# Optimization experiments

Measured on AMD Instinct MI355X. Metric: run time of the kernel, lower is better.

## Reference

```python
import jax, jax.numpy as jnp
import numpy as np
from jax import lax

N, T, E, A, D, S, O = 64, 2048, 512, 256, 512, 64, 80
R_ATT, R_FAC = 10, 2
H4 = 4 * D  # LSTM hidden size = 2048


def softsign(x):
    return x / (1.0 + jnp.abs(x))


def lstm_cell(x, h, c, Wih, Whh, bih, bhh):
    gates = x @ Wih.T + bih + h @ Whh.T + bhh
    i, f, g, o = jnp.split(gates, 4, axis=-1)  # torch gate order i,f,g,o
    c_new = jax.nn.sigmoid(f) * c + jax.nn.sigmoid(i) * jnp.tanh(g)
    h_new = jax.nn.sigmoid(o) * jnp.tanh(c_new)
    return h_new, c_new


def setup_inputs() -> dict:
    key = jax.random.key(0)
    ks = jax.random.split(key, 24)
    f = lambda k, shape, s=0.05: jax.random.normal(k, shape, dtype=jnp.float32) * s
    return {
        'input_enc': f(ks[0], (N, T, E), 1.0),
        'input_dec': f(ks[1], (N, O), 1.0),
        'spkr_vec': f(ks[2], (N, 1, S), 1.0),
        'speed': jax.random.uniform(ks[3], (N,), dtype=jnp.float32),
        'lengths_enc': jnp.full((N,), T, dtype=jnp.int32),
        'We': f(ks[4], (E, A)), 'be': jnp.zeros((A,), jnp.float32),
        'Ws': f(ks[5], (S, A)),
        'conv_w': f(ks[6], (A, 1, 31)),
        'w_proj': f(ks[7], (A,)), 'b_proj': jnp.zeros((), jnp.float32),
        'W_speed': f(ks[8], (A,)),
        'sp_W1': f(ks[9], (D,)), 'sp_b1': jnp.zeros((D,), jnp.float32),
        'sp_W2': f(ks[10], (D, E)), 'sp_b2': jnp.zeros((E,), jnp.float32),
        'pre_W1': f(ks[11], (O + S, 2 * D)), 'pre_b1': jnp.zeros((2 * D,), jnp.float32),
        'pre_W2': f(ks[12], (2 * D, D)), 'pre_b2': jnp.zeros((D,), jnp.float32),
        'Wih0': f(ks[13], (4 * H4, E + D + S)), 'Whh0': f(ks[14], (4 * H4, H4)),
        'bih0': jnp.zeros((4 * H4,), jnp.float32), 'bhh0': jnp.zeros((4 * H4,), jnp.float32),
        'Wih1': f(ks[15], (4 * H4, H4)), 'Whh1': f(ks[16], (4 * H4, H4)),
        'bih1': jnp.zeros((4 * H4,), jnp.float32), 'bhh1': jnp.zeros((4 * H4,), jnp.float32),
        'Wo': f(ks[17], (H4 + E, O * R_FAC)), 'bo': jnp.zeros((O * R_FAC,), jnp.float32),
    }


def _forward(input_enc, input_dec, spkr_vec, speed, lengths_enc,
             We, be, Ws, conv_w, w_proj, b_proj, W_speed,
             sp_W1, sp_b1, sp_W2, sp_b2,
             pre_W1, pre_b1, pre_W2, pre_b2,
             Wih0, Whh0, bih0, bhh0, Wih1, Whh1, bih1, bhh1, Wo, bo):
    n, t_enc, _ = input_enc.shape
    # first decoding step: previous attention = one-hot at t=0
    att0 = jnp.zeros((n, t_enc), jnp.float32).at[:, 0].set(1.0)
    bias_speed = (speed[:, None] * W_speed[None, :])[:, None, :]            # (N,1,A)
    bias_enc = softsign(jnp.einsum('nte,ea->nta', input_enc, We) + be)      # (N,T,A)
    bias_spkr = softsign(jnp.einsum('nse,ea->nsa', spkr_vec, Ws))           # (N,1,A)
    # prenet (dropout = identity at inference)
    x = jnp.concatenate([input_dec, spkr_vec[:, 0, :]], axis=-1)
    p = jax.nn.relu(jax.nn.relu(x @ pre_W1 + pre_b1) @ pre_W2 + pre_b2)     # (N,D)
    out_prenet = p[:, None, :]
    # location feature: conv1d(1->A, k=31, pad=15) over previous attention
    conv = lax.conv_general_dilated(att0[:, None, :], conv_w, (1,), [(15, 15)],
                                    dimension_numbers=('NCH', 'OIH', 'NCH'))
    conv = conv.transpose(0, 2, 1)                                          # (N,T,A)
    e = bias_enc + bias_spkr + conv + bias_speed                            # (N,T,A)
    # sliding-window mask around previous argmax, indices clamped to [0, len-1]
    m = jnp.argmax(att0, axis=1)                                            # (N,)
    L1 = (lengths_enc - 1).astype(m.dtype)
    i = jnp.arange(R_ATT)
    up = jnp.minimum(m[:, None] + i, L1[:, None])
    lo = jnp.minimum(jnp.maximum(m[:, None] - i, 0), L1[:, None])
    idx = jnp.concatenate([up, lo], axis=1)                                 # (N,2R)
    mask = jnp.zeros((n, t_enc), jnp.float32).at[jnp.arange(n)[:, None], idx].set(1.0)
    logit = jnp.einsum('nta,a->nt', jnp.tanh(e), w_proj) + b_proj           # (N,T)
    w = jnp.exp(logit - jnp.max(logit, axis=1, keepdims=True)) * mask
    att = w / jnp.maximum(jnp.sum(w, axis=1, keepdims=True), 1e-12)         # L1 normalize
    # speed-conditioned encoder shift
    sp = jnp.tanh(jax.nn.relu(speed[:, None] * sp_W1 + sp_b1) @ sp_W2 + sp_b2)  # (N,E)
    enc = input_enc + sp[:, None, :]
    context = jnp.einsum('nt,nte->ne', att, enc)[:, None, :]                # (N,1,E)
    in_lstm = jnp.concatenate([out_prenet, context, spkr_vec], axis=2)[:, 0, :]
    h0 = jnp.zeros((n, H4), jnp.float32)
    h1, _ = lstm_cell(in_lstm, h0, h0, Wih0, Whh0, bih0, bhh0)
    h2, _ = lstm_cell(h1, h0, h0, Wih1, Whh1, bih1, bhh1)
    dec_output = jnp.concatenate([h2[:, None, :], context], axis=2)         # (N,1,H4+E)
    output = (dec_output @ Wo + bo).reshape(n, R_FAC, -1)                   # (N,r,O)
    return output, context, dec_output


def reference(input_enc, input_dec, spkr_vec, speed, lengths_enc,
              We, be, Ws, conv_w, w_proj, b_proj, W_speed,
              sp_W1, sp_b1, sp_W2, sp_b2,
              pre_W1, pre_b1, pre_W2, pre_b2,
              Wih0, Whh0, bih0, bhh0, Wih1, Whh1, bih1, bhh1, Wo, bo):
    return _forward(input_enc, input_dec, spkr_vec, speed, lengths_enc,
                    We, be, Ws, conv_w, w_proj, b_proj, W_speed,
                    sp_W1, sp_b1, sp_W2, sp_b2,
                    pre_W1, pre_b1, pre_W2, pre_b2,
                    Wih0, Whh0, bih0, bhh0, Wih1, Whh1, bih1, bhh1, Wo, bo)
```

## Files before the change

### kernel.cpp

```cpp
#include <hip/hip_runtime.h>
#include <math.h>


__device__ __forceinline__ float sigmoidf_(float x){ return 1.0f/(1.0f+expf(-x)); }
__device__ __forceinline__ float softsignf_(float x){ return x/(1.0f+fabsf(x)); }


__global__ void hidden_kernel(const float* __restrict__ input_dec, const float* __restrict__ spkr,
                              const float* __restrict__ W, const float* __restrict__ b,
                              float* __restrict__ hid)
{
    const int n = blockIdx.x;
    const int j = blockIdx.y * 256 + threadIdx.x;
    float a0=0.f, a1=0.f, a2=0.f, a3=0.f;
    #pragma unroll 4
    for (int k = 0; k < 144; k += 4) {
        const float x0 = (k+0 < 80) ? input_dec[n*80 + k+0] : spkr[n*64 + (k+0-80)];
        const float x1 = (k+1 < 80) ? input_dec[n*80 + k+1] : spkr[n*64 + (k+1-80)];
        const float x2 = (k+2 < 80) ? input_dec[n*80 + k+2] : spkr[n*64 + (k+2-80)];
        const float x3 = (k+3 < 80) ? input_dec[n*80 + k+3] : spkr[n*64 + (k+3-80)];
        a0 = fmaf(x0, W[(k+0)*1024 + j], a0);
        a1 = fmaf(x1, W[(k+1)*1024 + j], a1);
        a2 = fmaf(x2, W[(k+2)*1024 + j], a2);
        a3 = fmaf(x3, W[(k+3)*1024 + j], a3);
    }
    hid[n*1024 + j] = fmaxf((a0+a1)+(a2+a3) + b[j], 0.f);
}

__global__ void sp_kernel(const float* __restrict__ speed, const float* __restrict__ sp_W1,
                          const float* __restrict__ sp_b1, const float* __restrict__ sp_W2,
                          const float* __restrict__ sp_b2, float* __restrict__ sp)
{
    const int n = blockIdx.x;
    const int j = blockIdx.y * 256 + threadIdx.x;
    const float s = speed[n];
    float a0=0.f, a1=0.f, a2=0.f, a3=0.f;
    #pragma unroll 4
    for (int d = 0; d < 512; d += 4) {
        const float r0 = fmaxf(fmaf(s, sp_W1[d+0], sp_b1[d+0]), 0.f);
        const float r1 = fmaxf(fmaf(s, sp_W1[d+1], sp_b1[d+1]), 0.f);
        const float r2 = fmaxf(fmaf(s, sp_W1[d+2], sp_b1[d+2]), 0.f);
        const float r3 = fmaxf(fmaf(s, sp_W1[d+3], sp_b1[d+3]), 0.f);
        a0 = fmaf(r0, sp_W2[(d+0)*512 + j], a0);
        a1 = fmaf(r1, sp_W2[(d+1)*512 + j], a1);
        a2 = fmaf(r2, sp_W2[(d+2)*512 + j], a2);
        a3 = fmaf(r3, sp_W2[(d+3)*512 + j], a3);
    }
    sp[n*512 + j] = tanhf((a0+a1)+(a2+a3) + sp_b2[j]);
}

__global__ void p_kernel(const float* __restrict__ hid, const float* __restrict__ W,
                         const float* __restrict__ b, float* __restrict__ xT0)
{
    const int n = blockIdx.x;
    const int j = blockIdx.y * 256 + threadIdx.x;
    const float* xr = hid + n*1024;
    float a0=0.f, a1=0.f, a2=0.f, a3=0.f;
    #pragma unroll 4
    for (int k = 0; k < 1024; k += 4) {
        a0 = fmaf(xr[k+0], W[(k+0)*512 + j], a0);
        a1 = fmaf(xr[k+1], W[(k+1)*512 + j], a1);
        a2 = fmaf(xr[k+2], W[(k+2)*512 + j], a2);
        a3 = fmaf(xr[k+3], W[(k+3)*512 + j], a3);
    }
    xT0[j*64 + n] = fmaxf((a0+a1)+(a2+a3) + b[j], 0.f);
}

__global__ void attn_kernel(const float* __restrict__ input_enc,
                            const float* __restrict__ spkr,
                            const float* __restrict__ speed,
                            const int*   __restrict__ lengths,
                            const float* __restrict__ We,
                            const float* __restrict__ be,
                            const float* __restrict__ Ws,
                            const float* __restrict__ conv_w,
                            const float* __restrict__ w_proj,
                            const float* __restrict__ b_proj,
                            const float* __restrict__ W_speed,
                            const float* __restrict__ sp,
                            float* __restrict__ xT0,
                            float* __restrict__ out_ctx,
                            float* __restrict__ out_dec)
{
    const int n = blockIdx.x;
    const int a = threadIdx.x;
    __shared__ float encs[10*512];
    __shared__ float part[4][10];
    __shared__ float logit_s[10];
    __shared__ float att_s[10];

    const int L1 = lengths[n] - 1;
    const int tc = (L1 + 1 < 10) ? (L1 + 1) : 10;
    const float sn = speed[n];
    const float* enc_n = input_enc + (size_t)n * (2048*512);

    for (int idx = a; idx < 10*512; idx += 256) encs[idx] = enc_n[idx];
    __syncthreads();

    float ds = 0.f;
    for (int s = 0; s < 64; ++s) ds = fmaf(spkr[n*64 + s], Ws[s*256 + a], ds);
    const float bspkr = softsignf_(ds);
    const float bspd  = sn * W_speed[a];
    const float bea   = be[a];
    const float wpa   = w_proj[a];

    float dt[10];
    #pragma unroll
    for (int t = 0; t < 10; ++t) dt[t] = 0.f;
    for (int k = 0; k < 512; ++k) {
        const float w = We[k*256 + a];
        #pragma unroll
        for (int t = 0; t < 10; ++t) dt[t] = fmaf(encs[t*512 + k], w, dt[t]);
    }

    for (int t = 0; t < 10; ++t) {
        float e = softsignf_(dt[t] + bea);
        e += bspkr + conv_w[a*31 + (15 - t)] + bspd;
        float v = tanhf(e) * wpa;
        #pragma unroll
        for (int off = 32; off > 0; off >>= 1) v += __shfl_down(v, off);
        if ((a & 63) == 0) part[a >> 6][t] = v;
    }
    __syncthreads();
    if (a < 10) logit_s[a] = part[0][a] + part[1][a] + part[2][a] + part[3][a] + b_proj[0];
    __syncthreads();
    if (a == 0) {
        float mx = -1e30f;
        for (int t = 0; t < tc; ++t) mx = fmaxf(mx, logit_s[t]);
        float ssum = 0.f;
        for (int t = 0; t < tc; ++t) { att_s[t] = expf(logit_s[t] - mx); ssum += att_s[t]; }
        const float inv = 1.f / fmaxf(ssum, 1e-12f);
        for (int t = 0; t < tc; ++t) att_s[t] *= inv;
        for (int t = tc; t < 10; ++t) att_s[t] = 0.f;
    }
    __syncthreads();

    for (int e0 = a; e0 < 512; e0 += 256) {
        const float spv = sp[n*512 + e0];
        float c = 0.f;
        for (int t = 0; t < tc; ++t) c = fmaf(att_s[t], encs[t*512 + e0] + spv, c);
        xT0[(512 + e0)*64 + n] = c;
        out_ctx[n*512 + e0]   = c;
        out_dec[n*2560 + 2048 + e0] = c;
    }
    if (a < 64) xT0[(1024 + a)*64 + n] = spkr[n*64 + a];
}

template<int K, bool FSKIP>
__global__ void gemm_big(const float* __restrict__ xT, const float* __restrict__ W,
                         const float* __restrict__ b1, const float* __restrict__ b2,
                         float* __restrict__ outT)
{
    const int tid = threadIdx.x;
    const int n = tid & 63;
    const int wv = __builtin_amdgcn_readfirstlane(tid >> 6);
    const int jj0 = blockIdx.x * 8 + wv * 4;
    const int j0  = (FSKIP && jj0 >= 2048) ? jj0 + 2048 : jj0;
    const float* Wr = W + (size_t)j0 * K;
    float acc0 = 0.f, acc1 = 0.f, acc2 = 0.f, acc3 = 0.f;
    #pragma unroll 2
    for (int k = 0; k < K; k += 4) {
        const float x0 = xT[(k+0)*64 + n];
        const float x1 = xT[(k+1)*64 + n];
        const float x2 = xT[(k+2)*64 + n];
        const float x3 = xT[(k+3)*64 + n];
        const float4 w0 = *reinterpret_cast<const float4*>(Wr + (size_t)0*K + k);
        const float4 w1 = *reinterpret_cast<const float4*>(Wr + (size_t)1*K + k);
        const float4 w2 = *reinterpret_cast<const float4*>(Wr + (size_t)2*K + k);
        const float4 w3 = *reinterpret_cast<const float4*>(Wr + (size_t)3*K + k);
        acc0 = fmaf(x3, w0.w, fmaf(x2, w0.z, fmaf(x1, w0.y, fmaf(x0, w0.x, acc0))));
        acc1 = fmaf(x3, w1.w, fmaf(x2, w1.z, fmaf(x1, w1.y, fmaf(x0, w1.x, acc1))));
        acc2 = fmaf(x3, w2.w, fmaf(x2, w2.z, fmaf(x1, w2.y, fmaf(x0, w2.x, acc2))));
        acc3 = fmaf(x3, w3.w, fmaf(x2, w3.z, fmaf(x1, w3.y, fmaf(x0, w3.x, acc3))));
    }
    acc0 += b1[j0+0] + b2[j0+0];
    acc1 += b1[j0+1] + b2[j0+1];
    acc2 += b1[j0+2] + b2[j0+2];
    acc3 += b1[j0+3] + b2[j0+3];
    outT[(jj0+0)*64 + n] = acc0;
    outT[(jj0+1)*64 + n] = acc1;
    outT[(jj0+2)*64 + n] = acc2;
    outT[(jj0+3)*64 + n] = acc3;
}

__global__ void lstm_act_kernel(const float* __restrict__ gT, float* __restrict__ hT,
                                float* __restrict__ dec_out)
{
    const int idx = blockIdx.x * 256 + threadIdx.x;
    const int n = idx & 63;
    const int m = idx >> 6;
    const float gi = gT[idx];
    const float gg = gT[2048*64 + idx];
    const float go = gT[4096*64 + idx];
    const float c = sigmoidf_(gi) * tanhf(gg);
    const float h = sigmoidf_(go) * tanhf(c);
    hT[idx] = h;
    if (dec_out) dec_out[n*2560 + m] = h;
}

__global__ void final_partial_kernel(const float* __restrict__ h2T, const float* __restrict__ ctx,
                                     const float* __restrict__ Wo, float* __restrict__ part)
{
    const int n  = blockIdx.x;
    const int kc = blockIdx.y;
    const int j  = threadIdx.x;
    if (j >= 160) return;
    const int k0 = kc * 128;
    float a0=0.f, a1=0.f, a2=0.f, a3=0.f;
    if (kc < 16) {
        #pragma unroll 4
        for (int k = k0; k < k0 + 128; k += 4) {
            a0 = fmaf(h2T[(k+0)*64 + n], Wo[(k+0)*160 + j], a0);
            a1 = fmaf(h2T[(k+1)*64 + n], Wo[(k+1)*160 + j], a1);
            a2 = fmaf(h2T[(k+2)*64 + n], Wo[(k+2)*160 + j], a2);
            a3 = fmaf(h2T[(k+3)*64 + n], Wo[(k+3)*160 + j], a3);
        }
    } else {
        const float* cr = ctx + n*512;
        #pragma unroll 4
        for (int k = k0; k < k0 + 128; k += 4) {
            a0 = fmaf(cr[k+0-2048], Wo[(k+0)*160 + j], a0);
            a1 = fmaf(cr[k+1-2048], Wo[(k+1)*160 + j], a1);
            a2 = fmaf(cr[k+2-2048], Wo[(k+2)*160 + j], a2);
            a3 = fmaf(cr[k+3-2048], Wo[(k+3)*160 + j], a3);
        }
    }
    part[(kc*64 + n)*160 + j] = (a0+a1)+(a2+a3);
}

__global__ void final_reduce_kernel(const float* __restrict__ part, const float* __restrict__ bo,
                                    float* __restrict__ out)
{
    const int idx = blockIdx.x * 256 + threadIdx.x;
    const int j = idx - (idx / 160) * 160;
    float s = bo[j];
    #pragma unroll
    for (int kc = 0; kc < 20; ++kc) s += part[kc*10240 + idx];
    out[idx] = s;
}

extern "C" void kernel_launch(void* const* d_in, const int* in_sizes, int n_in,
                              void* d_out, int out_size, void* d_ws, size_t ws_size,
                              hipStream_t stream)
{
    const float* input_enc = (const float*)d_in[0];
    const float* input_dec = (const float*)d_in[1];
    const float* spkr      = (const float*)d_in[2];
    const float* speed     = (const float*)d_in[3];
    const int*   lengths   = (const int*)  d_in[4];
    const float* We        = (const float*)d_in[5];
    const float* be        = (const float*)d_in[6];
    const float* Ws        = (const float*)d_in[7];
    const float* conv_w    = (const float*)d_in[8];
    const float* w_proj    = (const float*)d_in[9];
    const float* b_proj    = (const float*)d_in[10];
    const float* W_speed   = (const float*)d_in[11];
    const float* sp_W1     = (const float*)d_in[12];
    const float* sp_b1     = (const float*)d_in[13];
    const float* sp_W2     = (const float*)d_in[14];
    const float* sp_b2     = (const float*)d_in[15];
    const float* pre_W1    = (const float*)d_in[16];
    const float* pre_b1    = (const float*)d_in[17];
    const float* pre_W2    = (const float*)d_in[18];
    const float* pre_b2    = (const float*)d_in[19];
    const float* Wih0      = (const float*)d_in[20];
    const float* bih0      = (const float*)d_in[22];
    const float* bhh0      = (const float*)d_in[23];
    const float* Wih1      = (const float*)d_in[24];
    const float* bih1      = (const float*)d_in[26];
    const float* bhh1      = (const float*)d_in[27];
    const float* Wo        = (const float*)d_in[28];
    const float* bo        = (const float*)d_in[29];

    float* ws  = (float*)d_ws;
    float* XT0 = ws;
    float* G   = ws + 69632;
    float* XT1 = ws + 462848;
    float* HID = ws + 593920;
    float* SP  = ws + 659456;
    float* PART= ws + 69632;

    float* out     = (float*)d_out;
    float* out_ctx = out + 10240;
    float* out_dec = out + 43008;

    hidden_kernel<<<dim3(64,4), 256, 0, stream>>>(input_dec, spkr, pre_W1, pre_b1, HID);
    sp_kernel<<<dim3(64,2), 256, 0, stream>>>(speed, sp_W1, sp_b1, sp_W2, sp_b2, SP);
    p_kernel<<<dim3(64,2), 256, 0, stream>>>(HID, pre_W2, pre_b2, XT0);
    attn_kernel<<<64, 256, 0, stream>>>(input_enc, spkr, speed, lengths, We, be, Ws, conv_w,
                                        w_proj, b_proj, W_speed, SP, XT0, out_ctx, out_dec);
    gemm_big<1088, true><<<768, 128, 0, stream>>>(XT0, Wih0, bih0, bhh0, G);
    lstm_act_kernel<<<512, 256, 0, stream>>>(G, XT1, nullptr);
    gemm_big<2048, true><<<768, 128, 0, stream>>>(XT1, Wih1, bih1, bhh1, G);
    lstm_act_kernel<<<512, 256, 0, stream>>>(G, XT1, out_dec);
    final_partial_kernel<<<dim3(64,20), 256, 0, stream>>>(XT1, out_ctx, Wo, PART);
    final_reduce_kernel<<<40, 256, 0, stream>>>(PART, bo, out);
}
```

Measured before the change: 824.8 us.

## Replace per-wave GEMV-style gate GEMM with LDS-tiled split-K GEMM

```diff
diff --git a/kernel.cpp b/kernel.cpp
--- a/kernel.cpp
+++ b/kernel.cpp
@@ -4,6 +4,13 @@
 
 __device__ __forceinline__ float sigmoidf_(float x){ return 1.0f/(1.0f+expf(-x)); }
 __device__ __forceinline__ float softsignf_(float x){ return x/(1.0f+fabsf(x)); }
+
+__device__ __forceinline__ void llds16(const float* g, float* l)
+{
+    __builtin_amdgcn_global_load_lds(
+        (const __attribute__((address_space(1))) unsigned int*)g,
+        (__attribute__((address_space(3))) unsigned int*)l, 16, 0, 0);
+}
 
 
 __global__ void hidden_kernel(const float* __restrict__ input_dec, const float* __restrict__ spkr,
@@ -146,52 +153,101 @@
     if (a < 64) xT0[(1024 + a)*64 + n] = spkr[n*64 + a];
 }
 
-template<int K, bool FSKIP>
-__global__ void gemm_big(const float* __restrict__ xT, const float* __restrict__ W,
-                         const float* __restrict__ b1, const float* __restrict__ b2,
-                         float* __restrict__ outT)
-{
-    const int tid = threadIdx.x;
-    const int n = tid & 63;
-    const int wv = __builtin_amdgcn_readfirstlane(tid >> 6);
-    const int jj0 = blockIdx.x * 8 + wv * 4;
-    const int j0  = (FSKIP && jj0 >= 2048) ? jj0 + 2048 : jj0;
-    const float* Wr = W + (size_t)j0 * K;
-    float acc0 = 0.f, acc1 = 0.f, acc2 = 0.f, acc3 = 0.f;
-    #pragma unroll 2
-    for (int k = 0; k < K; k += 4) {
-        const float x0 = xT[(k+0)*64 + n];
-        const float x1 = xT[(k+1)*64 + n];
-        const float x2 = xT[(k+2)*64 + n];
-        const float x3 = xT[(k+3)*64 + n];
-        const float4 w0 = *reinterpret_cast<const float4*>(Wr + (size_t)0*K + k);
-        const float4 w1 = *reinterpret_cast<const float4*>(Wr + (size_t)1*K + k);
-        const float4 w2 = *reinterpret_cast<const float4*>(Wr + (size_t)2*K + k);
-        const float4 w3 = *reinterpret_cast<const float4*>(Wr + (size_t)3*K + k);
-        acc0 = fmaf(x3, w0.w, fmaf(x2, w0.z, fmaf(x1, w0.y, fmaf(x0, w0.x, acc0))));
-        acc1 = fmaf(x3, w1.w, fmaf(x2, w1.z, fmaf(x1, w1.y, fmaf(x0, w1.x, acc1))));
-        acc2 = fmaf(x3, w2.w, fmaf(x2, w2.z, fmaf(x1, w2.y, fmaf(x0, w2.x, acc2))));
-        acc3 = fmaf(x3, w3.w, fmaf(x2, w3.z, fmaf(x1, w3.y, fmaf(x0, w3.x, acc3))));
-    }
-    acc0 += b1[j0+0] + b2[j0+0];
-    acc1 += b1[j0+1] + b2[j0+1];
-    acc2 += b1[j0+2] + b2[j0+2];
-    acc3 += b1[j0+3] + b2[j0+3];
-    outT[(jj0+0)*64 + n] = acc0;
-    outT[(jj0+1)*64 + n] = acc1;
-    outT[(jj0+2)*64 + n] = acc2;
-    outT[(jj0+3)*64 + n] = acc3;
-}
-
-__global__ void lstm_act_kernel(const float* __restrict__ gT, float* __restrict__ hT,
-                                float* __restrict__ dec_out)
+#define FMA_ROW(acc, wv) do { \
+    acc.x = fmaf(wv.x, xk0.x, acc.x); acc.y = fmaf(wv.x, xk0.y, acc.y); \
+    acc.z = fmaf(wv.x, xk0.z, acc.z); acc.w = fmaf(wv.x, xk0.w, acc.w); \
+    acc.x = fmaf(wv.y, xk1.x, acc.x); acc.y = fmaf(wv.y, xk1.y, acc.y); \
+    acc.z = fmaf(wv.y, xk1.z, acc.z); acc.w = fmaf(wv.y, xk1.w, acc.w); \
+    acc.x = fmaf(wv.z, xk2.x, acc.x); acc.y = fmaf(wv.z, xk2.y, acc.y); \
+    acc.z = fmaf(wv.z, xk2.z, acc.z); acc.w = fmaf(wv.z, xk2.w, acc.w); \
+    acc.x = fmaf(wv.w, xk3.x, acc.x); acc.y = fmaf(wv.w, xk3.y, acc.y); \
+    acc.z = fmaf(wv.w, xk3.z, acc.z); acc.w = fmaf(wv.w, xk3.w, acc.w); \
+} while(0)
+
+template<int K>
+__global__ __launch_bounds__(256, 2)
+void gemm_tile(const float* __restrict__ xT, const float* __restrict__ W,
+               float* __restrict__ part)
+{
+    __shared__ __align__(16) float Wl[2][64*64];
+    __shared__ __align__(16) float Xl[2][64*64];
+    const int tid  = threadIdx.x;
+    const int lane = tid & 63;
+    const int w    = tid >> 6;
+    const int tx   = tid & 15;
+    const int ty   = tid >> 4;
+    const int jjbase = blockIdx.x * 64;
+    const int sy     = blockIdx.y;
+    const int jg     = jjbase + ((jjbase >= 2048) ? 2048 : 0);
+
+    constexpr int NT = K / 64;
+    constexpr int NTQ = NT / 4, NTR = NT % 4;
+    const int tn = NTQ + (sy < NTR ? 1 : 0);
+    const int t0 = sy * NTQ + (sy < NTR ? sy : NTR);
+
+    float4 a0 = {0,0,0,0}, a1 = {0,0,0,0}, a2 = {0,0,0,0}, a3 = {0,0,0,0};
+
+    auto stage = [&](int t, int b) {
+        const int k0 = t * 64;
+        #pragma unroll
+        for (int c = 0; c < 4; ++c) {
+            const int u = w * 4 + c;
+            llds16(xT + (size_t)k0 * 64 + u * 256 + lane * 4, &Xl[b][u * 256]);
+            const int r0 = u * 4;
+            llds16(W + (size_t)(jg + r0 + (lane >> 4)) * K + k0 + (lane & 15) * 4,
+                   &Wl[b][r0 * 64]);
+        }
+    };
+
+    stage(t0, 0);
+    __syncthreads();
+
+    for (int tt = 0; tt < tn; ++tt) {
+        const int cur = tt & 1;
+        if (tt + 1 < tn) stage(t0 + tt + 1, cur ^ 1);
+        const float* Wc = Wl[cur];
+        const float* Xc = Xl[cur];
+        #pragma unroll
+        for (int kk = 0; kk < 64; kk += 4) {
+            const float4 xk0 = *(const float4*)(Xc + (kk+0)*64 + tx*4);
+            const float4 xk1 = *(const float4*)(Xc + (kk+1)*64 + tx*4);
+            const float4 xk2 = *(const float4*)(Xc + (kk+2)*64 + tx*4);
+            const float4 xk3 = *(const float4*)(Xc + (kk+3)*64 + tx*4);
+            const float4 w0 = *(const float4*)(Wc + (ty*4+0)*64 + kk);
+            FMA_ROW(a0, w0);
+            const float4 w1 = *(const float4*)(Wc + (ty*4+1)*64 + kk);
+            FMA_ROW(a1, w1);
+            const float4 w2 = *(const float4*)(Wc + (ty*4+2)*64 + kk);
+            FMA_ROW(a2, w2);
+            const float4 w3 = *(const float4*)(Wc + (ty*4+3)*64 + kk);
+            FMA_ROW(a3, w3);
+        }
+        __syncthreads();
+    }
+
+    float* op = part + (size_t)(sy * 6144 + jjbase) * 64;
+    *(float4*)(op + (ty*4+0)*64 + tx*4) = a0;
+    *(float4*)(op + (ty*4+1)*64 + tx*4) = a1;
+    *(float4*)(op + (ty*4+2)*64 + tx*4) = a2;
+    *(float4*)(op + (ty*4+3)*64 + tx*4) = a3;
+}
+
+__global__ void lstm_act_kernel(const float* __restrict__ part,
+                                const float* __restrict__ b1, const float* __restrict__ b2,
+                                float* __restrict__ hT, float* __restrict__ dec_out)
 {
     const int idx = blockIdx.x * 256 + threadIdx.x;
     const int n = idx & 63;
     const int m = idx >> 6;
-    const float gi = gT[idx];
-    const float gg = gT[2048*64 + idx];
-    const float go = gT[4096*64 + idx];
+    float gi = b1[m]        + b2[m];
+    float gg = b1[4096 + m] + b2[4096 + m];
+    float go = b1[6144 + m] + b2[6144 + m];
+    #pragma unroll
+    for (int s = 0; s < 4; ++s) {
+        gi += part[(size_t)(s * 6144 +        m) * 64 + n];
+        gg += part[(size_t)(s * 6144 + 2048 + m) * 64 + n];
+        go += part[(size_t)(s * 6144 + 4096 + m) * 64 + n];
+    }
     const float c = sigmoidf_(gi) * tanhf(gg);
     const float h = sigmoidf_(go) * tanhf(c);
     hT[idx] = h;
@@ -273,12 +329,12 @@
     const float* bo        = (const float*)d_in[29];
 
     float* ws  = (float*)d_ws;
-    float* XT0 = ws;
-    float* G   = ws + 69632;
-    float* XT1 = ws + 462848;
-    float* HID = ws + 593920;
-    float* SP  = ws + 659456;
-    float* PART= ws + 69632;
+    float* XT0  = ws;
+    float* PART = ws + 69632;
+    float* XT1  = ws + 1642496;
+    float* HID  = ws + 1773568;
+    float* SP   = ws + 1839104;
+    float* FPART= ws + 69632;
 
     float* out     = (float*)d_out;
     float* out_ctx = out + 10240;
@@ -289,10 +345,10 @@
     p_kernel<<<dim3(64,2), 256, 0, stream>>>(HID, pre_W2, pre_b2, XT0);
     attn_kernel<<<64, 256, 0, stream>>>(input_enc, spkr, speed, lengths, We, be, Ws, conv_w,
                                         w_proj, b_proj, W_speed, SP, XT0, out_ctx, out_dec);
-    gemm_big<1088, true><<<768, 128, 0, stream>>>(XT0, Wih0, bih0, bhh0, G);
-    lstm_act_kernel<<<512, 256, 0, stream>>>(G, XT1, nullptr);
-    gemm_big<2048, true><<<768, 128, 0, stream>>>(XT1, Wih1, bih1, bhh1, G);
-    lstm_act_kernel<<<512, 256, 0, stream>>>(G, XT1, out_dec);
-    final_partial_kernel<<<dim3(64,20), 256, 0, stream>>>(XT1, out_ctx, Wo, PART);
-    final_reduce_kernel<<<40, 256, 0, stream>>>(PART, bo, out);
-}
+    gemm_tile<1088><<<dim3(96,4), 256, 0, stream>>>(XT0, Wih0, PART);
+    lstm_act_kernel<<<512, 256, 0, stream>>>(PART, bih0, bhh0, XT1, nullptr);
+    gemm_tile<2048><<<dim3(96,4), 256, 0, stream>>>(XT1, Wih1, PART);
+    lstm_act_kernel<<<512, 256, 0, stream>>>(PART, bih1, bhh1, XT1, out_dec);
+    final_partial_kernel<<<dim3(64,20), 256, 0, stream>>>(XT1, out_ctx, Wo, FPART);
+    final_reduce_kernel<<<40, 256, 0, stream>>>(FPART, bo, out);
+}
```

Result: faster. 668.6 us (-18.9%).
